# Performance work log

Measured on AMD Instinct MI355X. Metric: run time of the kernel, lower is better.

Reference implementation:

```python
import jax, jax.numpy as jnp
import numpy as np

HEADS = 8

def conv2d(x, w, b=None, pad=0, groups=1):
    y = jax.lax.conv_general_dilated(
        x, w, window_strides=(1, 1), padding=[(pad, pad), (pad, pad)],
        dimension_numbers=('NCHW', 'OIHW', 'NCHW'), feature_group_count=groups)
    if b is not None:
        y = y + b[None, :, None, None]
    return y

def l2norm(t, eps=1e-12):
    return t / jnp.maximum(jnp.linalg.norm(t, axis=-1, keepdims=True), eps)

def attention(x, y, temp, kv_w, kv_dw, q_w, q_dw, proj_w):
    b, c, h, w = x.shape
    kv = conv2d(conv2d(y, kv_w), kv_dw, pad=1, groups=2 * c)
    k, v = jnp.split(kv, 2, axis=1)
    q = conv2d(conv2d(x, q_w), q_dw, pad=1, groups=c)
    def resh(t):
        return t.reshape(b, HEADS, c // HEADS, h * w)
    q, k, v = resh(q), resh(k), resh(v)
    q, k = l2norm(q), l2norm(k)
    attn = jnp.einsum('bhcn,bhdn->bhcd', q, k) * temp  # [b,h,c/h,c/h]
    attn = jax.nn.softmax(attn, axis=-1)
    out = jnp.einsum('bhcd,bhdn->bhcn', attn, v).reshape(b, c, h, w)
    return conv2d(out, proj_w)

def resblock_l(x, w1, b1, w2, b2):
    h = jax.nn.relu(conv2d(x, w1, b1, pad=1))
    h = jax.nn.relu(conv2d(h, w2, b2, pad=1))
    return h + x

def resblock_g(x, w1, w2):
    _, _, H, W = x.shape
    y = jnp.fft.rfft2(x, axes=(-2, -1), norm='backward')
    yf = jnp.concatenate([y.real, y.imag], axis=1)  # [b,2c,H,W//2+1]
    yf = conv2d(jax.nn.relu(conv2d(yf, w1)), w2)
    yr, yi = jnp.split(yf, 2, axis=1)
    return jnp.fft.irfft2(yr + 1j * yi, s=(H, W), axes=(-2, -1), norm='backward')

def fuseblock(x0, x1, p):
    fre = resblock_l(x0, p['rl_w1'], p['rl_b1'], p['rl_w2'], p['rl_b2'])
    spa = resblock_g(x1, p['rg_w1'], p['rg_w2'])
    att = lambda a, b: attention(a, b, p['att_temp'], p['att_kv_w'], p['att_kv_dw'],
                                 p['att_q_w'], p['att_q_dw'], p['att_proj_w'])
    fre = att(fre, spa) + fre
    spa = att(spa, fre) + spa  # original reuses fre_att weights for both calls
    cat = jnp.concatenate([fre, spa], axis=1)
    c2 = cat.shape[1]
    g = conv2d(conv2d(cat, p['f1_dw'], p['f1_dwb'], pad=1, groups=c2), p['f1_pw'], p['f1_pwb'])
    c1 = g.shape[1]
    g = conv2d(conv2d(g, p['f2_dw'], p['f2_dwb'], pad=1, groups=c1), p['f2_pw'], p['f2_pwb'])
    g = jax.nn.sigmoid(g)
    fre_a, spa_a = jnp.split(g, 2, axis=1)
    res = fre * fre_a + spa_a * spa
    return jnp.nan_to_num(res, nan=1e-5, posinf=1e-5, neginf=1e-5)

def setup_inputs() -> dict:
    key = jax.random.key(0)
    C = 64
    B, H, W = 4, 256, 256
    ks = iter(jax.random.split(key, 32))
    n = lambda shape, s=0.02: (jax.random.normal(next(ks), shape, dtype=jnp.float32) * s)
    inp = {
        'x0': jax.random.normal(next(ks), (B, C, H, W), dtype=jnp.float32),
        'x1': jax.random.normal(next(ks), (B, C, H, W), dtype=jnp.float32),
        # ResBlock_L
        'rl_w1': n((C, C, 3, 3)), 'rl_b1': jnp.zeros((C,), jnp.float32),
        'rl_w2': n((C, C, 3, 3)), 'rl_b2': jnp.zeros((C,), jnp.float32),
        # ResBlock_G (1x1 convs on 2C channels, no bias)
        'rg_w1': n((2 * C, 2 * C, 1, 1)), 'rg_w2': n((2 * C, 2 * C, 1, 1)),
        # shared Attention (fre_att used twice)
        'att_temp': jnp.ones((HEADS, 1, 1), jnp.float32),
        'att_kv_w': n((2 * C, C, 1, 1)), 'att_kv_dw': n((2 * C, 1, 3, 3)),
        'att_q_w': n((C, C, 1, 1)), 'att_q_dw': n((C, 1, 3, 3)),
        'att_proj_w': n((C, C, 1, 1)),
        # fuse: DWConv(2C->C) then DWConv(C->2C)
        'f1_dw': n((2 * C, 1, 3, 3)), 'f1_dwb': jnp.zeros((2 * C,), jnp.float32),
        'f1_pw': n((C, 2 * C, 1, 1)), 'f1_pwb': jnp.zeros((C,), jnp.float32),
        'f2_dw': n((C, 1, 3, 3)), 'f2_dwb': jnp.zeros((C,), jnp.float32),
        'f2_pw': n((2 * C, C, 1, 1)), 'f2_pwb': jnp.zeros((2 * C,), jnp.float32),
    }
    return inp

def reference(x0, x1, rl_w1, rl_b1, rl_w2, rl_b2, rg_w1, rg_w2,
              att_temp, att_kv_w, att_kv_dw, att_q_w, att_q_dw, att_proj_w,
              f1_dw, f1_dwb, f1_pw, f1_pwb, f2_dw, f2_dwb, f2_pw, f2_pwb):
    p = dict(rl_w1=rl_w1, rl_b1=rl_b1, rl_w2=rl_w2, rl_b2=rl_b2,
             rg_w1=rg_w1, rg_w2=rg_w2, att_temp=att_temp, att_kv_w=att_kv_w,
             att_kv_dw=att_kv_dw, att_q_w=att_q_w, att_q_dw=att_q_dw,
             att_proj_w=att_proj_w, f1_dw=f1_dw, f1_dwb=f1_dwb, f1_pw=f1_pw,
             f1_pwb=f1_pwb, f2_dw=f2_dw, f2_dwb=f2_dwb, f2_pw=f2_pw, f2_pwb=f2_pwb)
    return fuseblock(x0, x1, p)
```

## Files before the change

### kernel.cpp

```cpp
#include <hip/hip_runtime.h>

#define HW 65536

typedef __attribute__((ext_vector_type(8))) _Float16 f16x8;
typedef __attribute__((ext_vector_type(4))) float floatx4;

__device__ inline unsigned short f2h(float f){
    return __builtin_bit_cast(unsigned short, (_Float16)f);
}
__device__ inline float h2f(unsigned short h){
    return (float)__builtin_bit_cast(_Float16, h);
}

__global__ void wprep_kernel(const float* __restrict__ w1, const float* __restrict__ w2,
                             unsigned short* __restrict__ wbf)
{
    int idx = blockIdx.x*256 + threadIdx.x;
    const float* src = (idx < 36864) ? w1 : w2;
    int l = idx % 36864;
    int ch = l / 18432;
    int r  = l % 18432;
    int tap = r >> 11;
    int co  = (r >> 5) & 63;
    int ci  = r & 31;
    wbf[idx] = f2h(src[co*576 + (ch*32+ci)*9 + tap]);
}

__global__ void wpack_kernel(const float* __restrict__ src, unsigned short* __restrict__ dst,
                             int CO, int CI)
{
    int idx = blockIdx.x*256 + threadIdx.x;
    if (idx >= CO*CI) return;
    int ci = idx % CI, co = idx / CI;
    dst[((size_t)(ci>>5)*CO + co)*32 + (ci&31)] = f2h(src[idx]);
}

__global__ __launch_bounds__(256,2)
void conv3x3_mfma_kernel(const float* __restrict__ in, const unsigned short* __restrict__ wbf,
                         const float* __restrict__ bias, const float* __restrict__ res,
                         float* __restrict__ out)
{
    __shared__ __align__(16) unsigned short s_in[6*66*72];
    const int t = threadIdx.x;
    const int lane = t & 63, wv = t >> 6;
    const int n = lane & 15, q = lane >> 4;
    const int blk = blockIdx.x;
    const int xt = blk & 3, yt = (blk>>2) & 63, b = blk >> 8;
    const int x0 = xt*64, y0 = yt*4;

    const float* inb = in + (size_t)b*64*HW;

    {
        const int xq = t & 15;
        const int u0 = t >> 4;
        const float* gp0 = inb + x0 + xq*4;
        float4 tmp[12];
        #pragma unroll
        for (int ch = 0; ch < 2; ch++) {
            #pragma unroll
            for (int i = 0; i < 12; i++) {
                int u = u0 + (ch*12 + i)*16;
                int ci = u & 63, row = u >> 6;
                int gy = y0 + row - 1;
                float4 v = make_float4(0.f,0.f,0.f,0.f);
                if (gy >= 0 && gy < 256)
                    v = *(const float4*)(gp0 + (size_t)ci*HW + (size_t)gy*256);
                tmp[i] = v;
            }
            #pragma unroll
            for (int i = 0; i < 12; i++) {
                int u = u0 + (ch*12 + i)*16;
                int ci = u & 63, row = u >> 6;
                unsigned short* d = &s_in[(row*66 + xq*4 + 1)*72 + ci];
                d[0]   = f2h(tmp[i].x);
                d[72]  = f2h(tmp[i].y);
                d[144] = f2h(tmp[i].z);
                d[216] = f2h(tmp[i].w);
            }
        }
        float hv[3];
        #pragma unroll
        for (int i = 0; i < 3; i++) {
            int idx = i*256 + t;
            int ci = idx & 63;
            int side = (idx >> 6) & 1;
            int row = idx >> 7;
            int gx = x0 - 1 + side*65;
            int gy = y0 + row - 1;
            float v = 0.f;
            if (gx >= 0 && gx < 256 && gy >= 0 && gy < 256)
                v = inb[(size_t)ci*HW + (size_t)gy*256 + gx];
            hv[i] = v;
        }
        #pragma unroll
        for (int i = 0; i < 3; i++) {
            int idx = i*256 + t;
            int ci = idx & 63;
            int side = (idx >> 6) & 1;
            int row = idx >> 7;
            int xx = side ? 65 : 0;
            s_in[(row*66 + xx)*72 + ci] = f2h(hv[i]);
        }
    }
    __syncthreads();

    floatx4 zero = {0.f,0.f,0.f,0.f};
    floatx4 acc[4][4];
    #pragma unroll
    for (int y=0;y<4;y++)
        #pragma unroll
        for (int s=0;s<4;s++) acc[y][s] = zero;

    for (int kk = 0; kk < 2; kk++) {
        f16x8 af[9];
        #pragma unroll
        for (int tap=0; tap<9; tap++)
            af[tap] = *(const f16x8*)&wbf[kk*18432 + tap*2048 + (wv*16 + n)*32 + q*8];
        #pragma unroll
        for (int s=0;s<4;s++){
            #pragma unroll
            for (int dx=0;dx<3;dx++){
                f16x8 bf[6];
                #pragma unroll
                for (int r6=0;r6<6;r6++)
                    bf[r6] = *(const f16x8*)&s_in[(r6*66 + s*16 + n + dx)*72 + kk*32 + q*8];
                #pragma unroll
                for (int dy=0;dy<3;dy++){
                    #pragma unroll
                    for (int y=0;y<4;y++)
                        acc[y][s] = __builtin_amdgcn_mfma_f32_16x16x32_f16(
                            af[dy*3+dx], bf[y+dy], acc[y][s], 0,0,0);
                }
            }
        }
    }

    #pragma unroll
    for (int y=0;y<4;y++){
        #pragma unroll
        for (int s=0;s<4;s++){
            #pragma unroll
            for (int r=0;r<4;r++){
                int co = wv*16 + q*4 + r;
                int px = x0 + s*16 + n;
                size_t off = ((size_t)b*64+co)*HW + (size_t)(y0+y)*256 + px;
                float v = fmaxf(acc[y][s][r] + bias[co], 0.f);
                if (res) v += res[off];
                out[off] = v;
            }
        }
    }
}

template<int MODE>
__global__ __launch_bounds__(256,2)
void pwdw_kernel(const float* __restrict__ in,
                 const unsigned short* __restrict__ wp, int wtot, int co_base,
                 const float* __restrict__ dww, int dw_choff,
                 float* __restrict__ outp,
                 const float* __restrict__ kin,
                 float* __restrict__ Gp,
                 float* __restrict__ kkv)
{
    __shared__ __align__(16) unsigned short s_buf[400*72];
    const int t = threadIdx.x;
    const int lane = t & 63, wv = t >> 6;
    const int n = lane & 15, q = lane >> 4;
    const int blk = blockIdx.x;
    const int xt = blk & 3, yt = (blk>>2) & 63, b = blk >> 8;
    const int x0 = xt*64, y0 = yt*4;
    const float* inb = in + (size_t)b*64*HW;

    {
        const int xq = t & 15;
        const int u0 = t >> 4;
        const float* gp0 = inb + x0 + xq*4;
        float4 tmp[12];
        #pragma unroll
        for (int ch = 0; ch < 2; ch++) {
            #pragma unroll
            for (int i = 0; i < 12; i++) {
                int u = u0 + (ch*12 + i)*16;
                int ci = u & 63, row = u >> 6;
                int gy = y0 + row - 1;
                float4 v = make_float4(0.f,0.f,0.f,0.f);
                if (gy >= 0 && gy < 256)
                    v = *(const float4*)(gp0 + (size_t)ci*HW + (size_t)gy*256);
                tmp[i] = v;
            }
            #pragma unroll
            for (int i = 0; i < 12; i++) {
                int u = u0 + (ch*12 + i)*16;
                int ci = u & 63, row = u >> 6;
                unsigned short* d = &s_buf[(row*66 + xq*4 + 1)*72 + ci];
                d[0]   = f2h(tmp[i].x);
                d[72]  = f2h(tmp[i].y);
                d[144] = f2h(tmp[i].z);
                d[216] = f2h(tmp[i].w);
            }
        }
        float hv[3];
        #pragma unroll
        for (int i = 0; i < 3; i++) {
            int idx = i*256 + t;
            int ci = idx & 63;
            int side = (idx >> 6) & 1;
            int row = idx >> 7;
            int gx = x0 - 1 + side*65;
            int gy = y0 + row - 1;
            float v = 0.f;
            if (gx >= 0 && gx < 256 && gy >= 0 && gy < 256)
                v = inb[(size_t)ci*HW + (size_t)gy*256 + gx];
            hv[i] = v;
        }
        #pragma unroll
        for (int i = 0; i < 3; i++) {
            int idx = i*256 + t;
            int ci = idx & 63;
            int side = (idx >> 6) & 1;
            int row = idx >> 7;
            int xx = side ? 65 : 0;
            s_buf[(row*66 + xx)*72 + ci] = f2h(hv[i]);
        }
    }
    __syncthreads();

    floatx4 zero = {0.f,0.f,0.f,0.f};
    floatx4 acc[25];
    #pragma unroll
    for (int g=0;g<25;g++) acc[g] = zero;
    f16x8 af[2];
    #pragma unroll
    for (int kk=0;kk<2;kk++)
        af[kk] = *(const f16x8*)&wp[((size_t)(kk*wtot + co_base + wv*16 + n))*32 + q*8];
    #pragma unroll
    for (int g=0;g<25;g++){
        #pragma unroll
        for (int kk=0;kk<2;kk++){
            f16x8 bf = *(const f16x8*)&s_buf[(g*16 + n)*72 + kk*32 + q*8];
            acc[g] = __builtin_amdgcn_mfma_f32_16x16x32_f16(af[kk], bf, acc[g], 0,0,0);
        }
    }
    __syncthreads();

    #pragma unroll
    for (int g=0;g<25;g++){
        #pragma unroll
        for (int r=0;r<4;r++)
            s_buf[(wv*16 + q*4 + r)*402 + g*16 + n] = f2h(acc[g][r]);
    }
    __syncthreads();

    const int co = t & 63, seg = t >> 6, x0l = seg*16;
    float w9[9];
    {
        const float* wpd = dww + (size_t)(dw_choff + co)*9;
        #pragma unroll
        for (int j=0;j<9;j++) w9[j] = wpd[j];
    }
    float gm[8];
    float qq_own = 0.f, kk_own = 0.f;
    if (MODE == 2){
        #pragma unroll
        for (int d=0;d<8;d++) gm[d] = 0.f;
    }
    const int base = lane & 56;

    #pragma unroll
    for (int yp=0; yp<2; yp++){
        float rwf[4][18];
        #pragma unroll
        for (int wr=0; wr<4; wr++){
            const unsigned* rp = (const unsigned*)&s_buf[co*402 + (yp*2+wr)*66 + x0l];
            #pragma unroll
            for (int j=0;j<9;j++){
                unsigned u = rp[j];
                rwf[wr][2*j]   = h2f((unsigned short)(u & 0xFFFFu));
                rwf[wr][2*j+1] = h2f((unsigned short)(u >> 16));
            }
        }
        #pragma unroll
        for (int yy=0; yy<2; yy++){
            float o[16];
            #pragma unroll
            for (int x=0;x<16;x++){
                float s = 0.f;
                #pragma unroll
                for (int dy=0;dy<3;dy++){
                    #pragma unroll
                    for (int dx=0;dx<3;dx++)
                        s = fmaf(w9[dy*3+dx], rwf[yy+dy][x+dx], s);
                }
                o[x] = s;
            }
            if (MODE == 0 || MODE == 1){
                size_t off = ((size_t)b*64 + co)*HW + (size_t)(y0 + yp*2 + yy)*256 + x0 + x0l;
                #pragma unroll
                for (int j=0;j<4;j++)
                    *(float4*)(outp + off + j*4) = make_float4(o[j*4],o[j*4+1],o[j*4+2],o[j*4+3]);
                if (MODE == 1){
                    #pragma unroll
                    for (int x=0;x<16;x++) kk_own = fmaf(o[x],o[x],kk_own);
                }
            } else {
                #pragma unroll
                for (int x=0;x<16;x++) qq_own = fmaf(o[x],o[x],qq_own);
                const float* kb = kin + ((size_t)b*64 + co)*HW + (size_t)(y0 + yp*2 + yy)*256 + x0 + x0l;
                float4 k4[4];
                #pragma unroll
                for (int j=0;j<4;j++) k4[j] = *(const float4*)(kb + j*4);
                #pragma unroll
                for (int d=0;d<8;d++){
                    #pragma unroll
                    for (int j=0;j<4;j++){
                        float kx = __shfl(k4[j].x, base+d);
                        float ky = __shfl(k4[j].y, base+d);
                        float kz = __shfl(k4[j].z, base+d);
                        float kw = __shfl(k4[j].w, base+d);
                        gm[d] = fmaf(o[j*4+0],kx,gm[d]);
                        gm[d] = fmaf(o[j*4+1],ky,gm[d]);
                        gm[d] = fmaf(o[j*4+2],kz,gm[d]);
                        gm[d] = fmaf(o[j*4+3],kw,gm[d]);
                    }
                }
            }
        }
    }

    if (MODE == 1){
        __syncthreads();
        float* redf = (float*)s_buf;
        redf[t] = kk_own;
        __syncthreads();
        if (t < 64){
            float s = redf[t] + redf[64+t] + redf[128+t] + redf[192+t];
            atomicAdd(&kkv[b*64 + t], s);
        }
    }
    if (MODE == 2){
        __syncthreads();
        float* redf = (float*)s_buf;
        #pragma unroll
        for (int d=0;d<8;d++) redf[seg*576 + co*9 + d] = gm[d];
        redf[seg*576 + co*9 + 8] = qq_own;
        __syncthreads();
        const int blkib = blk & 255;
        for (int i = t; i < 576; i += 256){
            float s = redf[i] + redf[576+i] + redf[1152+i] + redf[1728+i];
            int coi = i / 9, j = i - coi*9;
            if (j < 8) Gp[((size_t)b*576 + coi*8 + j)*256 + blkib] = s;
            else       Gp[((size_t)b*576 + 512 + coi)*256 + blkib] = s;
        }
    }
}

__global__ void gred_kernel(const float* __restrict__ Gp, float* __restrict__ G,
                            float* __restrict__ qq)
{
    int v = blockIdx.x*64 + threadIdx.x;
    if (v >= 2304) return;
    const float4* p = (const float4*)(Gp + (size_t)v*256);
    float s = 0.f;
    for (int j=0;j<64;j++){ float4 f = p[j]; s += f.x+f.y+f.z+f.w; }
    int b = v / 576, i = v - b*576;
    if (i < 512) G[(size_t)b*512 + i] = s;
    else         qq[(size_t)b*64 + (i-512)] = s;
}

template<int CIN, int COTILE>
__global__ __launch_bounds__(256,2)
void pw_mfma_kernel(const float* __restrict__ in, int in_cs, int in_choff,
                    float* __restrict__ out, int out_cs, int out_choff,
                    const unsigned short* __restrict__ wp, int wbstride, int wtot, int co_base,
                    const float* __restrict__ bias,
                    const float* __restrict__ res, int relu_flag, int P)
{
    constexpr int PXT   = (COTILE==32) ? 512 : (COTILE==64 ? 256 : 128);
    constexpr int HCO   = (COTILE==128) ? 2 : 1;
    constexpr int SCNT  = (PXT >= 256) ? 16 : 8;
    constexpr int NHALF = CIN/64;
    constexpr int NLD   = PXT*CIN/1024;
    constexpr int PXM   = PXT/4;

    __shared__ __align__(16) unsigned short s_a[NHALF][PXT*72];

    const int t = threadIdx.x;
    const int lane = t & 63, wv = t >> 6;
    const int n = lane & 15, q = lane >> 4;
    const int b = blockIdx.y;
    const int co_b = blockIdx.z * COTILE;
    const int p0 = blockIdx.x * PXT;
    const int colb   = (COTILE==32) ? (wv&1)*16 : wv*16;
    const int pxbase = (COTILE==32) ? (wv>>1)*256 : 0;

    const float* ipb = in + ((size_t)b*in_cs + in_choff)*P + p0;
    {
        float4 tmp[8];
        for (int c0 = 0; c0 < NLD; c0 += 8) {
            #pragma unroll
            for (int i=0;i<8;i++){
                int idx = t + (c0+i)*256;
                int px4 = idx & (PXM-1), ci = idx / PXM;
                tmp[i] = *(const float4*)(ipb + (size_t)ci*P + px4*4);
            }
            #pragma unroll
            for (int i=0;i<8;i++){
                int idx = t + (c0+i)*256;
                int px4 = idx & (PXM-1), ci = idx / PXM;
                unsigned short* d = &s_a[ci>>6][(px4*4)*72 + (ci&63)];
                d[0]   = f2h(tmp[i].x);
                d[72]  = f2h(tmp[i].y);
                d[144] = f2h(tmp[i].z);
                d[216] = f2h(tmp[i].w);
            }
        }
    }
    __syncthreads();

    floatx4 zero = {0.f,0.f,0.f,0.f};
    floatx4 acc[HCO][SCNT];
    #pragma unroll
    for (int h=0;h<HCO;h++)
        #pragma unroll
        for (int s=0;s<SCNT;s++) acc[h][s] = zero;

    f16x8 af[CIN/32][HCO];
    const unsigned short* wpb = wp + (size_t)b*wbstride;
    #pragma unroll
    for (int kk=0;kk<CIN/32;kk++)
        #pragma unroll
        for (int h=0;h<HCO;h++)
            af[kk][h] = *(const f16x8*)&wpb[((size_t)kk*wtot + co_b + h*64 + colb + n)*32 + q*8];

    #pragma unroll
    for (int s=0;s<SCNT;s++){
        #pragma unroll
        for (int kk=0;kk<CIN/32;kk++){
            f16x8 bf = *(const f16x8*)&s_a[kk>>1][(pxbase + s*16 + n)*72 + (kk&1)*32 + q*8];
            #pragma unroll
            for (int h=0;h<HCO;h++)
                acc[h][s] = __builtin_amdgcn_mfma_f32_16x16x32_f16(af[kk][h], bf, acc[h][s], 0,0,0);
        }
    }

    #pragma unroll
    for (int h=0;h<HCO;h++){
        #pragma unroll
        for (int s=0;s<SCNT;s++){
            int px = p0 + pxbase + s*16 + n;
            #pragma unroll
            for (int r=0;r<4;r++){
                int col = h*64 + colb + q*4 + r;
                size_t off = ((size_t)b*out_cs + out_choff + col)*P + px;
                float v = acc[h][s][r];
                if (bias) v += bias[col];
                if (relu_flag) v = fmaxf(v, 0.f);
                if (res) v += res[off];
                out[off] = v;
            }
        }
    }
}

__global__ __launch_bounds__(256,4)
void dw3x3_kernel(const float* __restrict__ in, int in_cs, int in_choff,
                  float* __restrict__ out, int out_cs, int out_choff,
                  const float* __restrict__ w, int w_choff,
                  const float* __restrict__ bias)
{
    const int c = blockIdx.x >> 6;
    const int p = ((blockIdx.x & 63) << 10) + threadIdx.x*4;
    const int x = p & 255, y = p >> 8;
    const int b = blockIdx.y;
    const float* ip = in + ((size_t)b*in_cs + in_choff + c)*HW;
    const float* wp = w + (size_t)(w_choff + c)*9;
    float row[3][6];
    #pragma unroll
    for (int dy=0; dy<3; dy++){
        int yy = y + dy - 1;
        if (yy < 0 || yy > 255){
            #pragma unroll
            for (int j=0;j<6;j++) row[dy][j]=0.f;
        } else {
            const float* rp = ip + yy*256;
            float4 m = *(const float4*)(rp + x);
            row[dy][1]=m.x; row[dy][2]=m.y; row[dy][3]=m.z; row[dy][4]=m.w;
            row[dy][0] = (x>0)   ? rp[x-1] : 0.f;
            row[dy][5] = (x<252) ? rp[x+4] : 0.f;
        }
    }
    float bv = bias ? bias[w_choff + c] : 0.f;
    float o[4] = {bv,bv,bv,bv};
    #pragma unroll
    for (int dy=0;dy<3;dy++){
        #pragma unroll
        for (int dx=0;dx<3;dx++){
            float wv = wp[dy*3+dx];
            #pragma unroll
            for (int i=0;i<4;i++) o[i] = fmaf(wv, row[dy][i+dx], o[i]);
        }
    }
    *(float4*)(out + ((size_t)b*out_cs + out_choff + c)*HW + p) =
        make_float4(o[0],o[1],o[2],o[3]);
}

__global__ __launch_bounds__(256,4)
void rfftw_kernel(const float* __restrict__ x, float* __restrict__ pm,
                  float* __restrict__ pe)
{
    __shared__ float sre[2*256], sim[2*256];
    const int t = threadIdx.x;
    const int r = t >> 7, lt = t & 127;
    const int row = blockIdx.x*2 + r;
    const int bc = row >> 8, h = row & 255;
    const float* xp = x + (size_t)bc*HW + h*256;
    float* base = sre + r*256; float* basei = sim + r*256;
    {
        int i1 = lt, i2 = lt + 128;
        int r1 = __brev((unsigned)i1) >> 24, r2 = __brev((unsigned)i2) >> 24;
        base[r1] = xp[i1]; basei[r1] = 0.f;
        base[r2] = xp[i2]; basei[r2] = 0.f;
    }
    __syncthreads();
    for (int s=1; s<=8; s++) {
        int m = 1<<s, half = m>>1;
        int j = lt & (half-1);
        int grp = lt >> (s-1);
        int i1 = grp*m + j, i2 = i1 + half;
        float ang = -6.283185307179586f * (float)j / (float)m;
        float sn, cs; __sincosf(ang, &sn, &cs);
        float ar = base[i1], ai = basei[i1];
        float br = base[i2], bi = basei[i2];
        float tr = cs*br - sn*bi, ti = cs*bi + sn*br;
        base[i1] = ar + tr; basei[i1] = ai + ti;
        base[i2] = ar - tr; basei[i2] = ai - ti;
        __syncthreads();
    }
    const int b = bc >> 6, c = bc & 63;
    float* pre = pm + ((size_t)b*128 + c)*32768 + h*128;
    float* pim = pm + ((size_t)b*128 + 64 + c)*32768 + h*128;
    pre[lt] = base[lt]; pim[lt] = basei[lt];
    if (lt == 0) {
        pe[((size_t)b*128 + c)*256 + h]      = base[128];
        pe[((size_t)b*128 + 64 + c)*256 + h] = basei[128];
    }
}

__global__ __launch_bounds__(256,2)
void ffth_kernel(float* __restrict__ pm, float* __restrict__ pe, int inverse)
{
    __shared__ float sre[256*16], sim[256*16];
    const int t = threadIdx.x;
    const int blk = blockIdx.x;
    const int chunk = blk % 9;
    const int bc = blk / 9;
    const int b = bc >> 6, c = bc & 63;
    const int col = t & 15;
    const int hb = t >> 4;
    const bool edge = (chunk == 8);
    const bool valid = edge ? (col == 0) : true;
    const int k = chunk*16 + col;
    float* pre; float* pim; int hstride;
    if (edge) {
        pre = pe + ((size_t)b*128 + c)*256;
        pim = pe + ((size_t)b*128 + 64 + c)*256;
        hstride = 1;
    } else {
        pre = pm + ((size_t)b*128 + c)*32768 + k;
        pim = pm + ((size_t)b*128 + 64 + c)*32768 + k;
        hstride = 128;
    }
    for (int hh = 0; hh < 16; hh++) {
        int h = hh*16 + hb;
        float vr = 0.f, vi = 0.f;
        if (valid) { vr = pre[h*hstride]; vi = pim[h*hstride]; }
        sre[h*16+col] = vr; sim[h*16+col] = vi;
    }
    __syncthreads();
    if (!inverse) {
        for (int s=8; s>=1; s--) {
            int m = 1<<s, half = m>>1;
            for (int it=0; it<8; it++) {
                int task = it*256 + t;
                int cl = task & 15;
                int bf = task >> 4;
                int j = bf & (half-1);
                int grp = bf >> (s-1);
                int i1 = grp*m + j, i2 = i1 + half;
                float ang = -6.283185307179586f * (float)j / (float)m;
                float sn, cs; __sincosf(ang, &sn, &cs);
                float ar = sre[i1*16+cl], ai = sim[i1*16+cl];
                float br = sre[i2*16+cl], bi = sim[i2*16+cl];
                float dr = ar - br, di = ai - bi;
                sre[i1*16+cl] = ar + br; sim[i1*16+cl] = ai + bi;
                sre[i2*16+cl] = cs*dr - sn*di;
                sim[i2*16+cl] = cs*di + sn*dr;
            }
            __syncthreads();
        }
    } else {
        for (int s=1; s<=8; s++) {
            int m = 1<<s, half = m>>1;
            for (int it=0; it<8; it++) {
                int task = it*256 + t;
                int cl = task & 15;
                int bf = task >> 4;
                int j = bf & (half-1);
                int grp = bf >> (s-1);
                int i1 = grp*m + j, i2 = i1 + half;
                float ang = 6.283185307179586f * (float)j / (float)m;
                float sn, cs; __sincosf(ang, &sn, &cs);
                float ar = sre[i1*16+cl], ai = sim[i1*16+cl];
                float br = sre[i2*16+cl], bi = sim[i2*16+cl];
                float tr = cs*br - sn*bi, ti = cs*bi + sn*br;
                sre[i1*16+cl] = ar + tr; sim[i1*16+cl] = ai + ti;
                sre[i2*16+cl] = ar - tr; sim[i2*16+cl] = ai - ti;
            }
            __syncthreads();
        }
    }
    const float scale = inverse ? (1.0f/256.0f) : 1.0f;
    for (int hh = 0; hh < 16; hh++) {
        int h = hh*16 + hb;
        if (valid) {
            pre[h*hstride] = sre[h*16+col]*scale;
            pim[h*hstride] = sim[h*16+col]*scale;
        }
    }
}

__global__ __launch_bounds__(256,4)
void irfftw_kernel(const float* __restrict__ pm, const float* __restrict__ pe,
                   float* __restrict__ outp)
{
    __shared__ float sre[2*256], sim[2*256];
    const int t = threadIdx.x;
    const int r = t >> 7, lt = t & 127;
    const int row = blockIdx.x*2 + r;
    const int bc = row >> 8, h = row & 255;
    const int b = bc >> 6, c = bc & 63;
    const float* pre = pm + ((size_t)b*128 + c)*32768 + h*128;
    const float* pim = pm + ((size_t)b*128 + 64 + c)*32768 + h*128;
    float* base = sre + r*256; float* basei = sim + r*256;
    {
        float xr = pre[lt], xi = pim[lt];
        int d1 = __brev((unsigned)lt) >> 24;
        base[d1] = xr; basei[d1] = xi;
        int k2 = lt + 128;
        int d2 = __brev((unsigned)k2) >> 24;
        float yr, yi;
        if (lt == 0) {
            yr = pe[((size_t)b*128 + c)*256 + h];
            yi = pe[((size_t)b*128 + 64 + c)*256 + h];
        } else {
            yr = pre[128-lt]; yi = -pim[128-lt];
        }
        base[d2] = yr; basei[d2] = yi;
    }
    __syncthreads();
    for (int s=1; s<=8; s++) {
        int m = 1<<s, half = m>>1;
        int j = lt & (half-1);
        int grp = lt >> (s-1);
        int i1 = grp*m + j, i2 = i1 + half;
        float ang = 6.283185307179586f * (float)j / (float)m;
        float sn, cs; __sincosf(ang, &sn, &cs);
        float ar = base[i1], ai = basei[i1];
        float br = base[i2], bi = basei[i2];
        float tr = cs*br - sn*bi, ti = cs*bi + sn*br;
        base[i1] = ar + tr; basei[i1] = ai + ti;
        base[i2] = ar - tr; basei[i2] = ai - ti;
        __syncthreads();
    }
    float* op = outp + (size_t)bc*HW + h*256;
    op[lt]     = base[lt]     * (1.0f/256.0f);
    op[lt+128] = base[lt+128] * (1.0f/256.0f);
}

__global__ void attnmat_kernel(const float* __restrict__ G, const float* __restrict__ qq,
                               const float* __restrict__ kk, const float* __restrict__ temp,
                               const float* __restrict__ projw, unsigned short* __restrict__ Mp)
{
    __shared__ float A[2048];
    const int t = threadIdx.x;
    for (int i = t; i < 2048; i += 256) {
        int d = i & 7, c = (i>>3)&7, bh = i>>6;
        int h = bh & 7;
        float nq = fmaxf(sqrtf(qq[bh*8+c]), 1e-12f);
        float nk = fmaxf(sqrtf(kk[bh*8+d]), 1e-12f);
        A[i] = G[i] / (nq*nk) * temp[h];
    }
    __syncthreads();
    {
        int base = t*8;
        float mx = -1e30f;
        #pragma unroll
        for (int d=0;d<8;d++) mx = fmaxf(mx, A[base+d]);
        float e[8]; float sum = 0.f;
        #pragma unroll
        for (int d=0;d<8;d++){ e[d] = __expf(A[base+d]-mx); sum += e[d]; }
        float inv = 1.0f/sum;
        #pragma unroll
        for (int d=0;d<8;d++) A[base+d] = e[d]*inv;
    }
    __syncthreads();
    for (int i=t; i<16384; i+=256) {
        int hd = i & 63, co = (i>>6)&63, b = i>>12;
        int h = hd>>3, d = hd&7;
        float s = 0.f;
        #pragma unroll
        for (int c=0;c<8;c++)
            s = fmaf(projw[co*64 + h*8 + c], A[((b*8+h)*8+c)*8 + d], s);
        Mp[(size_t)b*4096 + ((size_t)(hd>>5)*64 + co)*32 + (hd&31)] = f2h(s);
    }
}

__global__ __launch_bounds__(256,2)
void fuse_final_mfma_kernel(const float* __restrict__ t2, int t2_cs, int t2_choff,
                            const unsigned short* __restrict__ wp,
                            const float* __restrict__ bias,
                            const float* __restrict__ fre, const float* __restrict__ spa,
                            float* __restrict__ outp)
{
    __shared__ __align__(16) unsigned short s_a[128*72];
    const int t = threadIdx.x;
    const int lane = t & 63, wv = t >> 6;
    const int n = lane & 15, q = lane >> 4;
    const int b = blockIdx.y;
    const int p0 = blockIdx.x * 128;

    const float* ipb = t2 + ((size_t)b*t2_cs + t2_choff)*HW + p0;
    {
        float4 tmp[8];
        #pragma unroll
        for (int i=0;i<8;i++){
            int idx = t + i*256;
            int px4 = idx & 31, ci = idx >> 5;
            tmp[i] = *(const float4*)(ipb + (size_t)ci*HW + px4*4);
        }
        #pragma unroll
        for (int i=0;i<8;i++){
            int idx = t + i*256;
            int px4 = idx & 31, ci = idx >> 5;
            unsigned short* d = &s_a[(px4*4)*72 + ci];
            d[0]   = f2h(tmp[i].x);
            d[72]  = f2h(tmp[i].y);
            d[144] = f2h(tmp[i].z);
            d[216] = f2h(tmp[i].w);
        }
    }
    __syncthreads();

    floatx4 zero = {0.f,0.f,0.f,0.f};
    floatx4 acc[2][8];
    #pragma unroll
    for (int h=0;h<2;h++)
        #pragma unroll
        for (int s=0;s<8;s++) acc[h][s] = zero;

    f16x8 af[2][2];
    #pragma unroll
    for (int kk=0;kk<2;kk++)
        #pragma unroll
        for (int h=0;h<2;h++)
            af[kk][h] = *(const f16x8*)&wp[((size_t)kk*128 + h*64 + wv*16 + n)*32 + q*8];

    #pragma unroll
    for (int s=0;s<8;s++){
        #pragma unroll
        for (int kk=0;kk<2;kk++){
            f16x8 bf = *(const f16x8*)&s_a[(s*16 + n)*72 + kk*32 + q*8];
            #pragma unroll
            for (int h=0;h<2;h++)
                acc[h][s] = __builtin_amdgcn_mfma_f32_16x16x32_f16(af[kk][h], bf, acc[h][s], 0,0,0);
        }
    }

    #pragma unroll
    for (int s=0;s<8;s++){
        int px = p0 + s*16 + n;
        #pragma unroll
        for (int r=0;r<4;r++){
            int c = wv*16 + q*4 + r;
            float g1 = acc[0][s][r] + bias[c];
            float g2 = acc[1][s][r] + bias[64+c];
            float s1 = 1.0f/(1.0f+__expf(-g1));
            float s2 = 1.0f/(1.0f+__expf(-g2));
            size_t off = ((size_t)b*64 + c)*HW + px;
            float f = fre[off], sp = spa[off];
            float v = f*s1 + s2*sp;
            if (!__builtin_isfinite(v)) v = 1e-5f;
            outp[off] = v;
        }
    }
}

extern "C" void kernel_launch(void* const* d_in, const int* in_sizes, int n_in,
                              void* d_out, int out_size, void* d_ws, size_t ws_size,
                              hipStream_t stream) {
    const float* x0      = (const float*)d_in[0];
    const float* x1      = (const float*)d_in[1];
    const float* rl_w1   = (const float*)d_in[2];
    const float* rl_b1   = (const float*)d_in[3];
    const float* rl_w2   = (const float*)d_in[4];
    const float* rl_b2   = (const float*)d_in[5];
    const float* rg_w1   = (const float*)d_in[6];
    const float* rg_w2   = (const float*)d_in[7];
    const float* att_temp= (const float*)d_in[8];
    const float* kv_w    = (const float*)d_in[9];
    const float* kv_dw   = (const float*)d_in[10];
    const float* q_w     = (const float*)d_in[11];
    const float* q_dw    = (const float*)d_in[12];
    const float* proj_w  = (const float*)d_in[13];
    const float* f1_dw   = (const float*)d_in[14];
    const float* f1_dwb  = (const float*)d_in[15];
    const float* f1_pw   = (const float*)d_in[16];
    const float* f1_pwb  = (const float*)d_in[17];
    const float* f2_dw   = (const float*)d_in[18];
    const float* f2_dwb  = (const float*)d_in[19];
    const float* f2_pw   = (const float*)d_in[20];
    const float* f2_pwb  = (const float*)d_in[21];
    float* out = (float*)d_out;
    float* ws  = (float*)d_ws;

    const size_t A = (size_t)4*64*HW;
    float* R0   = ws;
    float* R1   = ws + A;
    float* spa  = ws + 2*A;
    float* PFe  = ws + 3*A;
    float* PFe2 = PFe + 131072;
    float* G    = PFe2 + 131072;
    float* qqv  = G + 2048;
    float* kkv  = qqv + 256;
    unsigned short* wbf = (unsigned short*)(kkv + 256);
    unsigned short* kvP = wbf + 2*36864;
    unsigned short* qP  = kvP + 8192;
    unsigned short* rg1P= qP  + 4096;
    unsigned short* rg2P= rg1P+ 16384;
    unsigned short* f1P = rg2P+ 16384;
    unsigned short* f2P = f1P + 8192;
    unsigned short* Mp  = f2P + 8192;
    float* fre  = out;

    const dim3 dwg64(64*64, 4);

    wprep_kernel<<<288,256,0,stream>>>(rl_w1, rl_w2, wbf);
    wpack_kernel<<<32,256,0,stream>>>(kv_w,  kvP, 128, 64);
    wpack_kernel<<<16,256,0,stream>>>(q_w,   qP,   64, 64);
    wpack_kernel<<<64,256,0,stream>>>(rg_w1, rg1P,128,128);
    wpack_kernel<<<64,256,0,stream>>>(rg_w2, rg2P,128,128);
    wpack_kernel<<<32,256,0,stream>>>(f1_pw, f1P,  64,128);
    wpack_kernel<<<32,256,0,stream>>>(f2_pw, f2P, 128, 64);

    conv3x3_mfma_kernel<<<1024,256,0,stream>>>(x0, wbf,         rl_b1, nullptr, R0);
    conv3x3_mfma_kernel<<<1024,256,0,stream>>>(R0, wbf + 36864, rl_b2, x0,      fre);

    rfftw_kernel<<<32768,256,0,stream>>>(x1, R0, PFe);
    ffth_kernel<<<2304,256,0,stream>>>(R0, PFe, 0);
    pw_mfma_kernel<128,128><<<dim3(256,4),256,0,stream>>>(R0,128,0,  R1,128,0,  rg1P,0,128,0, nullptr, nullptr, 1, 32768);
    pw_mfma_kernel<128,128><<<dim3(2,4),  256,0,stream>>>(PFe,128,0, PFe2,128,0, rg1P,0,128,0, nullptr, nullptr, 1, 256);
    pw_mfma_kernel<128,128><<<dim3(256,4),256,0,stream>>>(R1,128,0,  R0,128,0,  rg2P,0,128,0, nullptr, nullptr, 0, 32768);
    pw_mfma_kernel<128,128><<<dim3(2,4),  256,0,stream>>>(PFe2,128,0, PFe,128,0, rg2P,0,128,0, nullptr, nullptr, 0, 256);
    ffth_kernel<<<2304,256,0,stream>>>(R0, PFe, 1);
    irfftw_kernel<<<32768,256,0,stream>>>(R0, PFe, spa);

    auto attention = [&](const float* xq, const float* ykv, float* io) {
        hipMemsetAsync(G, 0, 2560*sizeof(float), stream);
        float* Gp = R0;
        pwdw_kernel<1><<<1024,256,0,stream>>>(ykv, kvP, 128, 0,  kv_dw, 0,
                                              R1, nullptr, nullptr, kkv);
        pwdw_kernel<2><<<1024,256,0,stream>>>(xq,  qP,  64,  0,  q_dw,  0,
                                              nullptr, R1, Gp, nullptr);
        gred_kernel<<<36,64,0,stream>>>(Gp, G, qqv);
        attnmat_kernel<<<1,256,0,stream>>>(G, qqv, kkv, att_temp, proj_w, Mp);
        pwdw_kernel<0><<<1024,256,0,stream>>>(ykv, kvP, 128, 64, kv_dw, 64,
                                              R0, nullptr, nullptr, nullptr);
        pw_mfma_kernel<64,64><<<dim3(256,4),256,0,stream>>>(R0,64,0, io,64,0, Mp,4096,64,0, nullptr, io, 0, HW);
    };
    attention(fre, spa, fre);
    attention(spa, fre, spa);

    float* W128 = R0;
    dw3x3_kernel<<<dwg64,256,0,stream>>>(fre,64,0, W128,128,0,  f1_dw, 0,  f1_dwb);
    dw3x3_kernel<<<dwg64,256,0,stream>>>(spa,64,0, W128,128,64, f1_dw, 64, f1_dwb);
    pw_mfma_kernel<128,64><<<dim3(256,4),256,0,stream>>>(W128,128,0, W128,128,0, f1P,0,64,0, f1_pwb, nullptr, 0, HW);
    dw3x3_kernel<<<dwg64,256,0,stream>>>(W128,128,0, W128,128,64, f2_dw, 0, f2_dwb);
    fuse_final_mfma_kernel<<<dim3(512,4),256,0,stream>>>(W128,128,64, f2P, f2_pwb, fre, spa, out);
    (void)in_sizes; (void)n_in; (void)out_size; (void)ws_size;
}
```

Before: 1.279 ms.

## Swizzle LDS layouts, fuse V-path pwdw with attention projection, merge weight prep

Applies an XOR swizzle to the fp16 LDS tiles in the conv3x3, pwdw, pw_mfma and final fuse kernels to reduce bank conflicts on the 16-byte MFMA operand reads. Adds a MODE 3 to pwdw that computes the V depthwise output, writes it back into shared memory, and applies the combined attention*projection matrix with MFMA plus the residual add in place. This removes the R0 round trip and the separate pw_mfma launch. The six weight-packing launches are also merged into one prep kernel. The fused mode adds two extra barriers and more register pressure.

Result: faster. 1.163 ms (-9.1%).

```diff
diff --git a/kernel.cpp b/kernel.cpp
--- a/kernel.cpp
+++ b/kernel.cpp
@@ -11,28 +11,42 @@
 __device__ inline float h2f(unsigned short h){
     return (float)__builtin_bit_cast(_Float16, h);
 }
-
-__global__ void wprep_kernel(const float* __restrict__ w1, const float* __restrict__ w2,
-                             unsigned short* __restrict__ wbf)
+__device__ inline int swz(int p, int ci){
+    return ci ^ (((p>>3)&7)<<3);
+}
+
+__global__ void prep_kernel(const float* __restrict__ w1, const float* __restrict__ w2,
+                            const float* __restrict__ kv_w, const float* __restrict__ q_w,
+                            const float* __restrict__ rg_w1, const float* __restrict__ rg_w2,
+                            const float* __restrict__ f1_pw, const float* __restrict__ f2_pw,
+                            unsigned short* __restrict__ wbf, unsigned short* __restrict__ kvP,
+                            unsigned short* __restrict__ qP, unsigned short* __restrict__ rg1P,
+                            unsigned short* __restrict__ rg2P, unsigned short* __restrict__ f1P,
+                            unsigned short* __restrict__ f2P)
 {
     int idx = blockIdx.x*256 + threadIdx.x;
-    const float* src = (idx < 36864) ? w1 : w2;
-    int l = idx % 36864;
-    int ch = l / 18432;
-    int r  = l % 18432;
-    int tap = r >> 11;
-    int co  = (r >> 5) & 63;
-    int ci  = r & 31;
-    wbf[idx] = f2h(src[co*576 + (ch*32+ci)*9 + tap]);
-}
-
-__global__ void wpack_kernel(const float* __restrict__ src, unsigned short* __restrict__ dst,
-                             int CO, int CI)
-{
-    int idx = blockIdx.x*256 + threadIdx.x;
-    if (idx >= CO*CI) return;
-    int ci = idx % CI, co = idx / CI;
-    dst[((size_t)(ci>>5)*CO + co)*32 + (ci&31)] = f2h(src[idx]);
+    if (idx < 73728) {
+        const float* src = (idx < 36864) ? w1 : w2;
+        int l = idx % 36864;
+        int ch = l / 18432;
+        int r  = l % 18432;
+        int tap = r >> 11;
+        int co  = (r >> 5) & 63;
+        int ci  = r & 31;
+        wbf[idx] = f2h(src[co*576 + (ch*32+ci)*9 + tap]);
+        return;
+    }
+    int i = idx - 73728;
+    const float* src; unsigned short* dst; int CI;
+    if (i < 8192)       { src=kv_w;  dst=kvP;  CI=64;  }
+    else if (i < 12288) { i-=8192;  src=q_w;   dst=qP;   CI=64;  }
+    else if (i < 28672) { i-=12288; src=rg_w1; dst=rg1P; CI=128; }
+    else if (i < 45056) { i-=28672; src=rg_w2; dst=rg2P; CI=128; }
+    else if (i < 53248) { i-=45056; src=f1_pw; dst=f1P;  CI=128; }
+    else                { i-=53248; src=f2_pw; dst=f2P;  CI=64;  }
+    int CO = (dst==qP || dst==f1P) ? 64 : 128;
+    int ci = i % CI, co = i / CI;
+    dst[((size_t)(ci>>5)*CO + co)*32 + (ci&31)] = f2h(src[i]);
 }
 
 __global__ __launch_bounds__(256,2)
@@ -71,11 +85,11 @@
             for (int i = 0; i < 12; i++) {
                 int u = u0 + (ch*12 + i)*16;
                 int ci = u & 63, row = u >> 6;
-                unsigned short* d = &s_in[(row*66 + xq*4 + 1)*72 + ci];
-                d[0]   = f2h(tmp[i].x);
-                d[72]  = f2h(tmp[i].y);
-                d[144] = f2h(tmp[i].z);
-                d[216] = f2h(tmp[i].w);
+                int pb = row*66 + xq*4 + 1;
+                s_in[(pb+0)*72 + swz(pb+0,ci)] = f2h(tmp[i].x);
+                s_in[(pb+1)*72 + swz(pb+1,ci)] = f2h(tmp[i].y);
+                s_in[(pb+2)*72 + swz(pb+2,ci)] = f2h(tmp[i].z);
+                s_in[(pb+3)*72 + swz(pb+3,ci)] = f2h(tmp[i].w);
             }
         }
         float hv[3];
@@ -99,7 +113,8 @@
             int side = (idx >> 6) & 1;
             int row = idx >> 7;
             int xx = side ? 65 : 0;
-            s_in[(row*66 + xx)*72 + ci] = f2h(hv[i]);
+            int p = row*66 + xx;
+            s_in[p*72 + swz(p,ci)] = f2h(hv[i]);
         }
     }
     __syncthreads();
@@ -122,8 +137,10 @@
             for (int dx=0;dx<3;dx++){
                 f16x8 bf[6];
                 #pragma unroll
-                for (int r6=0;r6<6;r6++)
-                    bf[r6] = *(const f16x8*)&s_in[(r6*66 + s*16 + n + dx)*72 + kk*32 + q*8];
+                for (int r6=0;r6<6;r6++){
+                    int p = r6*66 + s*16 + n + dx;
+                    bf[r6] = *(const f16x8*)&s_in[p*72 + ((((kk<<2)|q) ^ ((p>>3)&7))<<3)];
+                }
                 #pragma unroll
                 for (int dy=0;dy<3;dy++){
                     #pragma unroll
@@ -160,7 +177,8 @@
                  float* __restrict__ outp,
                  const float* __restrict__ kin,
                  float* __restrict__ Gp,
-                 float* __restrict__ kkv)
+                 float* __restrict__ kkv,
+                 const unsigned short* __restrict__ mw)
 {
     __shared__ __align__(16) unsigned short s_buf[400*72];
     const int t = threadIdx.x;
@@ -192,11 +210,11 @@
             for (int i = 0; i < 12; i++) {
                 int u = u0 + (ch*12 + i)*16;
                 int ci = u & 63, row = u >> 6;
-                unsigned short* d = &s_buf[(row*66 + xq*4 + 1)*72 + ci];
-                d[0]   = f2h(tmp[i].x);
-                d[72]  = f2h(tmp[i].y);
-                d[144] = f2h(tmp[i].z);
-                d[216] = f2h(tmp[i].w);
+                int pb = row*66 + xq*4 + 1;
+                s_buf[(pb+0)*72 + swz(pb+0,ci)] = f2h(tmp[i].x);
+                s_buf[(pb+1)*72 + swz(pb+1,ci)] = f2h(tmp[i].y);
+                s_buf[(pb+2)*72 + swz(pb+2,ci)] = f2h(tmp[i].z);
+                s_buf[(pb+3)*72 + swz(pb+3,ci)] = f2h(tmp[i].w);
             }
         }
         float hv[3];
@@ -220,7 +238,8 @@
             int side = (idx >> 6) & 1;
             int row = idx >> 7;
             int xx = side ? 65 : 0;
-            s_buf[(row*66 + xx)*72 + ci] = f2h(hv[i]);
+            int p = row*66 + xx;
+            s_buf[p*72 + swz(p,ci)] = f2h(hv[i]);
         }
     }
     __syncthreads();
@@ -235,9 +254,10 @@
         af[kk] = *(const f16x8*)&wp[((size_t)(kk*wtot + co_base + wv*16 + n))*32 + q*8];
     #pragma unroll
     for (int g=0;g<25;g++){
+        int p = g*16 + n;
         #pragma unroll
         for (int kk=0;kk<2;kk++){
-            f16x8 bf = *(const f16x8*)&s_buf[(g*16 + n)*72 + kk*32 + q*8];
+            f16x8 bf = *(const f16x8*)&s_buf[p*72 + ((((kk<<2)|q) ^ ((p>>3)&7))<<3)];
             acc[g] = __builtin_amdgcn_mfma_f32_16x16x32_f16(af[kk], bf, acc[g], 0,0,0);
         }
     }
@@ -258,6 +278,76 @@
         #pragma unroll
         for (int j=0;j<9;j++) w9[j] = wpd[j];
     }
+
+    if constexpr (MODE == 3) {
+        float o4[4][16];
+        #pragma unroll
+        for (int yp=0; yp<2; yp++){
+            float rwf[4][18];
+            #pragma unroll
+            for (int wr=0; wr<4; wr++){
+                const unsigned* rp = (const unsigned*)&s_buf[co*402 + (yp*2+wr)*66 + x0l];
+                #pragma unroll
+                for (int j=0;j<9;j++){
+                    unsigned u = rp[j];
+                    rwf[wr][2*j]   = h2f((unsigned short)(u & 0xFFFFu));
+                    rwf[wr][2*j+1] = h2f((unsigned short)(u >> 16));
+                }
+            }
+            #pragma unroll
+            for (int yy=0; yy<2; yy++){
+                #pragma unroll
+                for (int x=0;x<16;x++){
+                    float s = 0.f;
+                    #pragma unroll
+                    for (int dy=0;dy<3;dy++)
+                        #pragma unroll
+                        for (int dx=0;dx<3;dx++)
+                            s = fmaf(w9[dy*3+dx], rwf[yy+dy][x+dx], s);
+                    o4[yp*2+yy][x] = s;
+                }
+            }
+        }
+        __syncthreads();
+        #pragma unroll
+        for (int r4=0;r4<4;r4++){
+            #pragma unroll
+            for (int j=0;j<16;j++){
+                int pxl = r4*64 + x0l + j;
+                s_buf[pxl*72 + swz(pxl,co)] = f2h(o4[r4][j]);
+            }
+        }
+        __syncthreads();
+        f16x8 am[2];
+        #pragma unroll
+        for (int kk=0;kk<2;kk++)
+            am[kk] = *(const f16x8*)&mw[(size_t)b*4096 + ((size_t)kk*64 + wv*16 + n)*32 + q*8];
+        floatx4 accm[16];
+        #pragma unroll
+        for (int s=0;s<16;s++) accm[s] = zero;
+        #pragma unroll
+        for (int s=0;s<16;s++){
+            int p = s*16 + n;
+            #pragma unroll
+            for (int kk=0;kk<2;kk++){
+                f16x8 bf = *(const f16x8*)&s_buf[p*72 + ((((kk<<2)|q) ^ ((p>>3)&7))<<3)];
+                accm[s] = __builtin_amdgcn_mfma_f32_16x16x32_f16(am[kk], bf, accm[s], 0,0,0);
+            }
+        }
+        #pragma unroll
+        for (int s=0;s<16;s++){
+            int pxl = s*16 + n;
+            int yy = pxl >> 6, xx = pxl & 63;
+            #pragma unroll
+            for (int r=0;r<4;r++){
+                int coo = wv*16 + q*4 + r;
+                size_t off = ((size_t)b*64+coo)*HW + (size_t)(y0+yy)*256 + x0 + xx;
+                outp[off] = accm[s][r] + outp[off];
+            }
+        }
+        return;
+    }
+
     float gm[8];
     float qq_own = 0.f, kk_own = 0.f;
     if (MODE == 2){
@@ -293,15 +383,13 @@
                 }
                 o[x] = s;
             }
-            if (MODE == 0 || MODE == 1){
+            if (MODE == 1){
                 size_t off = ((size_t)b*64 + co)*HW + (size_t)(y0 + yp*2 + yy)*256 + x0 + x0l;
                 #pragma unroll
                 for (int j=0;j<4;j++)
                     *(float4*)(outp + off + j*4) = make_float4(o[j*4],o[j*4+1],o[j*4+2],o[j*4+3]);
-                if (MODE == 1){
-                    #pragma unroll
-                    for (int x=0;x<16;x++) kk_own = fmaf(o[x],o[x],kk_own);
-                }
+                #pragma unroll
+                for (int x=0;x<16;x++) kk_own = fmaf(o[x],o[x],kk_own);
             } else {
                 #pragma unroll
                 for (int x=0;x<16;x++) qq_own = fmaf(o[x],o[x],qq_own);
@@ -407,11 +495,12 @@
             for (int i=0;i<8;i++){
                 int idx = t + (c0+i)*256;
                 int px4 = idx & (PXM-1), ci = idx / PXM;
-                unsigned short* d = &s_a[ci>>6][(px4*4)*72 + (ci&63)];
-                d[0]   = f2h(tmp[i].x);
-                d[72]  = f2h(tmp[i].y);
-                d[144] = f2h(tmp[i].z);
-                d[216] = f2h(tmp[i].w);
+                int cih = ci & 63, half = ci >> 6;
+                int pb = px4*4;
+                s_a[half][(pb+0)*72 + swz(pb+0,cih)] = f2h(tmp[i].x);
+                s_a[half][(pb+1)*72 + swz(pb+1,cih)] = f2h(tmp[i].y);
+                s_a[half][(pb+2)*72 + swz(pb+2,cih)] = f2h(tmp[i].z);
+                s_a[half][(pb+3)*72 + swz(pb+3,cih)] = f2h(tmp[i].w);
             }
         }
     }
@@ -434,9 +523,10 @@
 
     #pragma unroll
     for (int s=0;s<SCNT;s++){
+        int p = pxbase + s*16 + n;
         #pragma unroll
         for (int kk=0;kk<CIN/32;kk++){
-            f16x8 bf = *(const f16x8*)&s_a[kk>>1][(pxbase + s*16 + n)*72 + (kk&1)*32 + q*8];
+            f16x8 bf = *(const f16x8*)&s_a[kk>>1][p*72 + (((((kk&1)<<2)|q) ^ ((p>>3)&7))<<3)];
             #pragma unroll
             for (int h=0;h<HCO;h++)
                 acc[h][s] = __builtin_amdgcn_mfma_f32_16x16x32_f16(af[kk][h], bf, acc[h][s], 0,0,0);
@@ -742,11 +832,11 @@
         for (int i=0;i<8;i++){
             int idx = t + i*256;
             int px4 = idx & 31, ci = idx >> 5;
-            unsigned short* d = &s_a[(px4*4)*72 + ci];
-            d[0]   = f2h(tmp[i].x);
-            d[72]  = f2h(tmp[i].y);
-            d[144] = f2h(tmp[i].z);
-            d[216] = f2h(tmp[i].w);
+            int pb = px4*4;
+            s_a[(pb+0)*72 + swz(pb+0,ci)] = f2h(tmp[i].x);
+            s_a[(pb+1)*72 + swz(pb+1,ci)] = f2h(tmp[i].y);
+            s_a[(pb+2)*72 + swz(pb+2,ci)] = f2h(tmp[i].z);
+            s_a[(pb+3)*72 + swz(pb+3,ci)] = f2h(tmp[i].w);
         }
     }
     __syncthreads();
@@ -767,9 +857,10 @@
 
     #pragma unroll
     for (int s=0;s<8;s++){
+        int p = s*16 + n;
         #pragma unroll
         for (int kk=0;kk<2;kk++){
-            f16x8 bf = *(const f16x8*)&s_a[(s*16 + n)*72 + kk*32 + q*8];
+            f16x8 bf = *(const f16x8*)&s_a[p*72 + ((((kk<<2)|q) ^ ((p>>3)&7))<<3)];
             #pragma unroll
             for (int h=0;h<2;h++)
                 acc[h][s] = __builtin_amdgcn_mfma_f32_16x16x32_f16(af[kk][h], bf, acc[h][s], 0,0,0);
@@ -844,13 +935,9 @@
 
     const dim3 dwg64(64*64, 4);
 
-    wprep_kernel<<<288,256,0,stream>>>(rl_w1, rl_w2, wbf);
-    wpack_kernel<<<32,256,0,stream>>>(kv_w,  kvP, 128, 64);
-    wpack_kernel<<<16,256,0,stream>>>(q_w,   qP,   64, 64);
-    wpack_kernel<<<64,256,0,stream>>>(rg_w1, rg1P,128,128);
-    wpack_kernel<<<64,256,0,stream>>>(rg_w2, rg2P,128,128);
-    wpack_kernel<<<32,256,0,stream>>>(f1_pw, f1P,  64,128);
-    wpack_kernel<<<32,256,0,stream>>>(f2_pw, f2P, 128, 64);
+    prep_kernel<<<528,256,0,stream>>>(rl_w1, rl_w2, kv_w, q_w, rg_w1, rg_w2,
+                                      f1_pw, f2_pw,
+                                      wbf, kvP, qP, rg1P, rg2P, f1P, f2P);
 
     conv3x3_mfma_kernel<<<1024,256,0,stream>>>(x0, wbf,         rl_b1, nullptr, R0);
     conv3x3_mfma_kernel<<<1024,256,0,stream>>>(R0, wbf + 36864, rl_b2, x0,      fre);
@@ -868,14 +955,13 @@
         hipMemsetAsync(G, 0, 2560*sizeof(float), stream);
         float* Gp = R0;
         pwdw_kernel<1><<<1024,256,0,stream>>>(ykv, kvP, 128, 0,  kv_dw, 0,
-                                              R1, nullptr, nullptr, kkv);
+                                              R1, nullptr, nullptr, kkv, nullptr);
         pwdw_kernel<2><<<1024,256,0,stream>>>(xq,  qP,  64,  0,  q_dw,  0,
-                                              nullptr, R1, Gp, nullptr);
+                                              nullptr, R1, Gp, nullptr, nullptr);
         gred_kernel<<<36,64,0,stream>>>(Gp, G, qqv);
         attnmat_kernel<<<1,256,0,stream>>>(G, qqv, kkv, att_temp, proj_w, Mp);
-        pwdw_kernel<0><<<1024,256,0,stream>>>(ykv, kvP, 128, 64, kv_dw, 64,
-                                              R0, nullptr, nullptr, nullptr);
-        pw_mfma_kernel<64,64><<<dim3(256,4),256,0,stream>>>(R0,64,0, io,64,0, Mp,4096,64,0, nullptr, io, 0, HW);
+        pwdw_kernel<3><<<1024,256,0,stream>>>(ykv, kvP, 128, 64, kv_dw, 64,
+                                              io, nullptr, nullptr, nullptr, Mp);
     };
     attention(fre, spa, fre);
     attention(spa, fre, spa);
```
